# Kernel optimization log

Measured on AMD Instinct MI355X. Metric: run time of the kernel, lower is better.

## Reference

```python
import jax, jax.numpy as jnp
import numpy as np

B, T, IN = 1048576, 4, 2
SPIN, TRAIN = 1000, 500000  # spinLen, traintimeLen


def setup_inputs() -> dict:
    key = jax.random.key(0)
    ks = jax.random.split(key, 5)
    return {
        "x": jax.random.normal(ks[0], (B, T, IN), jnp.float32),
        "y_obs": jax.random.normal(ks[1], (B, 1), jnp.float32),
        "weight_r_yom": jax.random.uniform(ks[2], (1, 1), jnp.float32),
        "weight_r_ylm": jax.random.uniform(ks[3], (1, 1), jnp.float32),
        "weight_r_yfm": jax.random.uniform(ks[4], (1, 1), jnp.float32),
        "epoch": 1,
        "time_lag": 0,
    }


def _forward(x, y_obs, wom, wlm, wfm, time_lag):
    # x: (B, T, 2) batch_first; module transposes and loops b (outer), t (inner)
    Bn, Tn, _ = x.shape
    # constant softmax-derived gates (hidden_size = 1 -> scalars)
    denom = jnp.exp(wom) + jnp.exp(wlm) + jnp.exp(wfm)
    oo = (jnp.exp(wom) / denom).reshape(())
    ol = (jnpp := jnp.exp(wlm) / denom).reshape(()) if False else (jnp.exp(wlm) / denom).reshape(())
    f = 1.0 - oo - ol
    # flattened linear recurrence: c_after[k] = f * c_after[k-1] + u[k], c_after[-1]=0
    u = x[time_lag:, :, 0].reshape(-1)  # ((B - time_lag) * T,)
    a = f * jnp.ones_like(u)

    def combine(e1, e2):
        a1, b1 = e1
        a2, b2 = e2
        return a1 * a2, a2 * b1 + b2

    _, c_after = jax.lax.associative_scan(combine, (a, u))
    c_before = jnp.concatenate([jnp.zeros((1,), u.dtype), c_after[:-1]])
    # the module records c_0 / h_0 / l_0 at the LAST t iteration of each b,
    # i.e., the carry just before step index (b - time_lag) * T + (T - 1)
    idx = jnp.arange(Bn - time_lag) * Tn + (Tn - 1)
    c0 = c_before[idx]  # (B - time_lag,)
    c0_full = jnp.concatenate([jnp.zeros((time_lag,), u.dtype), c0])[:, None]  # (B, 1)
    valid = (jnp.arange(Bn) >= time_lag)[:, None]  # rows < time_lag stay zero

    zeros = jnp.zeros((Bn, 1), u.dtype)
    c_n = c0_full                      # zero-padded already for b < time_lag
    q_n = oo * c0_full                 # h_0 (unused in outputs, kept for clarity)
    h_n = oo * c0_full                 # h_0 + bp_0, with bp_0 = 0 (ib = 0)
    l_n = ol * c0_full
    bp_n = zeros
    Gate_ib = zeros
    Gate_oo = jnp.where(valid, oo, 0.0).astype(u.dtype)
    Gate_ol = jnp.where(valid, ol, 0.0).astype(u.dtype)
    Gate_f = jnp.where(valid, f, 0.0).astype(u.dtype)
    obsstd = jnp.std(y_obs[SPIN:TRAIN], ddof=1)  # torch.std is unbiased
    obs_std = jnp.where(valid, obsstd, 0.0).astype(u.dtype)
    h_nout = jnp.concatenate([h_n, obs_std], axis=1)  # (B, 2)
    return (h_n, c_n, l_n, bp_n, Gate_ib, Gate_oo, Gate_ol, Gate_f, h_nout, obs_std)


def reference(x, y_obs, weight_r_yom, weight_r_ylm, weight_r_yfm, epoch, time_lag):
    del epoch  # unused by the module
    return _forward(x, y_obs, weight_r_yom, weight_r_ylm, weight_r_yfm, int(time_lag))
```

## Files before the change

### kernel.cpp

```cpp
#include <hip/hip_runtime.h>


#define SPIN 1000
#define TRAIN 500000
#define NPART 256

__global__ void __launch_bounds__(256)
reduce_partial_k(const float* __restrict__ y, int B, double* __restrict__ part) {
  const int hi = TRAIN < B ? TRAIN : B;
  const int q0 = SPIN / 4;
  const int q1 = hi / 4;
  float s = 0.f, s2 = 0.f;
  const float4* y4 = reinterpret_cast<const float4*>(y);
  for (int q = q0 + blockIdx.x * 256 + threadIdx.x; q < q1; q += NPART * 256) {
    float4 v = y4[q];
    s += v.x + v.y + v.z + v.w;
    s2 += v.x * v.x + v.y * v.y + v.z * v.z + v.w * v.w;
  }
  if (blockIdx.x == 0 && threadIdx.x == 0) {
    for (int i = q1 * 4; i < hi; ++i) { float v = y[i]; s += v; s2 += v * v; }
  }
  for (int off = 32; off; off >>= 1) {
    s += __shfl_down(s, off, 64);
    s2 += __shfl_down(s2, off, 64);
  }
  __shared__ float ls[4], ls2[4];
  const int t = threadIdx.x;
  if ((t & 63) == 0) { ls[t >> 6] = s; ls2[t >> 6] = s2; }
  __syncthreads();
  if (t == 0) {
    double S = 0, S2 = 0;
    for (int j = 0; j < 4; ++j) { S += ls[j]; S2 += ls2[j]; }
    part[2 * blockIdx.x] = S;
    part[2 * blockIdx.x + 1] = S2;
  }
}

__global__ void __launch_bounds__(256)
main_out_k(const float* __restrict__ x, const double* __restrict__ part,
           const float* __restrict__ wom, const float* __restrict__ wlm,
           const float* __restrict__ wfm, const int* __restrict__ tl_p,
           float* __restrict__ out, int B) {
  __shared__ float u[1088];
  __shared__ float scal[4];

  const int t = threadIdx.x;
  const int tl = tl_p[0];
  const int b0 = blockIdx.x * 256;
  const int i0 = b0 - tl;
  const int klo4 = 4 * (i0 - 16);
  const int X0 = tl * 8;

  for (int p = t; p < 544; p += 256) {
    int k = klo4 + 2 * p;
    float2 w = make_float2(0.f, 0.f);
    if (k >= 0) {
      float4 v = *reinterpret_cast<const float4*>(x + X0 + 2 * k);
      w = make_float2(v.x, v.z);
    }
    *reinterpret_cast<float2*>(&u[2 * p]) = w;
  }

  if (t < 64) {
    double S = 0, S2 = 0;
    for (int j = t; j < NPART; j += 64) { S += part[2 * j]; S2 += part[2 * j + 1]; }
    for (int m = 32; m; m >>= 1) {
      S += __shfl_xor(S, m, 64);
      S2 += __shfl_xor(S2, m, 64);
    }
    if (t == 0) {
      const int hi = TRAIN < B ? TRAIN : B;
      double n = (double)(hi - SPIN);
      double var = (S2 - S * S / n) / (n - 1.0);
      float sd = (float)sqrt(var > 0.0 ? var : 0.0);
      float eo = expf(wom[0]), el = expf(wlm[0]), ef = expf(wfm[0]);
      float denom = eo + el + ef;
      float oo = eo / denom, ol = el / denom;
      scal[0] = oo; scal[1] = ol; scal[2] = 1.f - oo - ol; scal[3] = sd;
    }
  }
  __syncthreads();

  const int b = b0 + t;
  if (b >= B) return;
  const float oo = scal[0], ol = scal[1], f = scal[2], sd = scal[3];
  const float f2 = f * f, f3 = f2 * f, f4 = f2 * f2;

  const float4* uq = reinterpret_cast<const float4*>(u);
  float c = uq[t].w;
#pragma unroll
  for (int m = 1; m <= 15; ++m) {
    float4 q = uq[t + m];
    float w = fmaf(fmaf(fmaf(q.x, f, q.y), f, q.z), f, q.w);
    c = fmaf(f4, c, w);
  }
  float4 qf = uq[t + 16];
  c = fmaf(f3, c, fmaf(fmaf(qf.x, f, qf.y), f, qf.z));

  const bool valid = (b >= tl);
  if (!valid) c = 0.f;
  const float h = oo * c;
  const float l = ol * c;
  const int Bl = B;
  out[b] = h;
  out[Bl + b] = c;
  out[2 * Bl + b] = l;
  out[3 * Bl + b] = 0.f;
  out[4 * Bl + b] = 0.f;
  out[5 * Bl + b] = valid ? oo : 0.f;
  out[6 * Bl + b] = valid ? ol : 0.f;
  out[7 * Bl + b] = valid ? f : 0.f;
  const float sdm = valid ? sd : 0.f;
  reinterpret_cast<float2*>(out + 8 * Bl)[b] = make_float2(h, sdm);
  out[10 * Bl + b] = sdm;
}

extern "C" void kernel_launch(void* const* d_in, const int* in_sizes, int n_in,
                              void* d_out, int out_size, void* d_ws,
                              size_t ws_size, hipStream_t stream) {
  const float* x = (const float*)d_in[0];
  const float* y_obs = (const float*)d_in[1];
  const float* wom = (const float*)d_in[2];
  const float* wlm = (const float*)d_in[3];
  const float* wfm = (const float*)d_in[4];
  const int* tl = (const int*)d_in[6];
  float* out = (float*)d_out;
  const int B = in_sizes[1];

  double* part = (double*)d_ws;

  reduce_partial_k<<<NPART, 256, 0, stream>>>(y_obs, B, part);
  const int grid = (B + 255) / 256;
  main_out_k<<<grid, 256, 0, stream>>>(x, part, wom, wlm, wfm, tl, out, B);
}
```

Before: 112.8 us.

## Move constant gate output writes into reduction kernel with vectorized stores

```diff
diff --git a/kernel.cpp b/kernel.cpp
--- a/kernel.cpp
+++ b/kernel.cpp
@@ -4,35 +4,62 @@
 #define SPIN 1000
 #define TRAIN 500000
 #define NPART 256
+#define G1 512
 
 __global__ void __launch_bounds__(256)
-reduce_partial_k(const float* __restrict__ y, int B, double* __restrict__ part) {
-  const int hi = TRAIN < B ? TRAIN : B;
-  const int q0 = SPIN / 4;
-  const int q1 = hi / 4;
-  float s = 0.f, s2 = 0.f;
-  const float4* y4 = reinterpret_cast<const float4*>(y);
-  for (int q = q0 + blockIdx.x * 256 + threadIdx.x; q < q1; q += NPART * 256) {
-    float4 v = y4[q];
-    s += v.x + v.y + v.z + v.w;
-    s2 += v.x * v.x + v.y * v.y + v.z * v.z + v.w * v.w;
+reduce_const_k(const float* __restrict__ y, int B, double* __restrict__ part,
+               const float* __restrict__ wom, const float* __restrict__ wlm,
+               const float* __restrict__ wfm, const int* __restrict__ tl_p,
+               float* __restrict__ out) {
+  const int t = threadIdx.x;
+
+  if (blockIdx.x < NPART) {
+    const int hi = TRAIN < B ? TRAIN : B;
+    const int q0 = SPIN / 4;
+    const int q1 = hi / 4;
+    float s = 0.f, s2 = 0.f;
+    const float4* y4 = reinterpret_cast<const float4*>(y);
+    for (int q = q0 + blockIdx.x * 256 + t; q < q1; q += NPART * 256) {
+      float4 v = y4[q];
+      s += v.x + v.y + v.z + v.w;
+      s2 += v.x * v.x + v.y * v.y + v.z * v.z + v.w * v.w;
+    }
+    if (blockIdx.x == 0 && t == 0) {
+      for (int i = q1 * 4; i < hi; ++i) { float v = y[i]; s += v; s2 += v * v; }
+    }
+    for (int off = 32; off; off >>= 1) {
+      s += __shfl_down(s, off, 64);
+      s2 += __shfl_down(s2, off, 64);
+    }
+    __shared__ float ls[4], ls2[4];
+    if ((t & 63) == 0) { ls[t >> 6] = s; ls2[t >> 6] = s2; }
+    __syncthreads();
+    if (t == 0) {
+      double S = 0, S2 = 0;
+      for (int j = 0; j < 4; ++j) { S += ls[j]; S2 += ls2[j]; }
+      part[2 * blockIdx.x] = S;
+      part[2 * blockIdx.x + 1] = S2;
+    }
   }
-  if (blockIdx.x == 0 && threadIdx.x == 0) {
-    for (int i = q1 * 4; i < hi; ++i) { float v = y[i]; s += v; s2 += v * v; }
-  }
-  for (int off = 32; off; off >>= 1) {
-    s += __shfl_down(s, off, 64);
-    s2 += __shfl_down(s2, off, 64);
-  }
-  __shared__ float ls[4], ls2[4];
-  const int t = threadIdx.x;
-  if ((t & 63) == 0) { ls[t >> 6] = s; ls2[t >> 6] = s2; }
-  __syncthreads();
-  if (t == 0) {
-    double S = 0, S2 = 0;
-    for (int j = 0; j < 4; ++j) { S += ls[j]; S2 += ls2[j]; }
-    part[2 * blockIdx.x] = S;
-    part[2 * blockIdx.x + 1] = S2;
+
+  const float eo = expf(wom[0]), el = expf(wlm[0]), ef = expf(wfm[0]);
+  const float denom = eo + el + ef;
+  const float oo = eo / denom, ol = el / denom;
+  const float f = 1.f - oo - ol;
+  const int tl = tl_p[0];
+  const int nq = B >> 2;
+  const int r3 = 3 * nq, r4 = 4 * nq, r5 = 5 * nq, r6 = 6 * nq, r7 = 7 * nq;
+  float4* out4 = reinterpret_cast<float4*>(out);
+  const float4 z = make_float4(0.f, 0.f, 0.f, 0.f);
+  for (int i = blockIdx.x * 256 + t; i < nq; i += G1 * 256) {
+    const int b = 4 * i;
+    float4 m = make_float4(b >= tl ? 1.f : 0.f, b + 1 >= tl ? 1.f : 0.f,
+                           b + 2 >= tl ? 1.f : 0.f, b + 3 >= tl ? 1.f : 0.f);
+    out4[r3 + i] = z;
+    out4[r4 + i] = z;
+    out4[r5 + i] = make_float4(oo * m.x, oo * m.y, oo * m.z, oo * m.w);
+    out4[r6 + i] = make_float4(ol * m.x, ol * m.y, ol * m.z, ol * m.w);
+    out4[r7 + i] = make_float4(f * m.x, f * m.y, f * m.z, f * m.w);
   }
 }
 
@@ -105,11 +132,6 @@
   out[b] = h;
   out[Bl + b] = c;
   out[2 * Bl + b] = l;
-  out[3 * Bl + b] = 0.f;
-  out[4 * Bl + b] = 0.f;
-  out[5 * Bl + b] = valid ? oo : 0.f;
-  out[6 * Bl + b] = valid ? ol : 0.f;
-  out[7 * Bl + b] = valid ? f : 0.f;
   const float sdm = valid ? sd : 0.f;
   reinterpret_cast<float2*>(out + 8 * Bl)[b] = make_float2(h, sdm);
   out[10 * Bl + b] = sdm;
@@ -129,7 +151,7 @@
 
   double* part = (double*)d_ws;
 
-  reduce_partial_k<<<NPART, 256, 0, stream>>>(y_obs, B, part);
+  reduce_const_k<<<G1, 256, 0, stream>>>(y_obs, B, part, wom, wlm, wfm, tl, out);
   const int grid = (B + 255) / 256;
   main_out_k<<<grid, 256, 0, stream>>>(x, part, wom, wlm, wfm, tl, out, B);
 }
```

Result: no change. 114.4 us (+1.5%).
